# Performance work log

Hardware: AMD Instinct MI355X
Metric: run time of the kernel (lower is better)

The kernel has to match this reference:

```python
import jax, jax.numpy as jnp
import numpy as np


def setup_inputs() -> dict:
    key = jax.random.key(0)
    ks = jax.random.split(key, 5)
    B, Tm1, N, H = 128, 255, 256, 256  # batch, t-1, input_size, hidden_encoder
    X = jax.random.normal(ks[0], (B, Tm1, N), dtype=jnp.float32)
    W_attn = jax.random.normal(ks[1], (2 * H + Tm1, 1), dtype=jnp.float32) * 0.05
    b_attn = jnp.zeros((1,), dtype=jnp.float32)
    W_lstm = jax.random.normal(ks[2], (N, 4 * H), dtype=jnp.float32) * 0.05
    U_lstm = jax.random.normal(ks[3], (H, 4 * H), dtype=jnp.float32) * 0.05
    b_lstm = jnp.zeros((4 * H,), dtype=jnp.float32)
    return {"X": X, "W_attn": W_attn, "b_attn": b_attn,
            "W_lstm": W_lstm, "U_lstm": U_lstm, "b_lstm": b_lstm}


def reference(X, W_attn, b_attn, W_lstm, U_lstm, b_lstm):
    B, Tm1, N = X.shape
    H = U_lstm.shape[0]
    # init_state: RepeatVector(H)(X[:,0,:])[:,:,0] == X[:,0,0] tiled across hidden
    h0 = jnp.broadcast_to(X[:, 0, 0:1], (B, H))
    c0 = h0
    Xp = jnp.transpose(X, (0, 2, 1))  # (B, N, Tm1), reused every step

    def step(carry, x_t):  # x_t: (B, N) = X[:, t, :]
        h, c = carry
        # encoder_concat: (B, N, 2H + Tm1)
        feat = jnp.concatenate([
            jnp.broadcast_to(h[:, None, :], (B, N, H)),
            jnp.broadcast_to(c[:, None, :], (B, N, H)),
            Xp,
        ], axis=2)
        e = jnp.einsum('bnf,fo->bno', feat, W_attn)[..., 0] + b_attn[0]  # (B, N)
        alpha = jax.nn.softmax(e, axis=-1)  # softmax over input_size
        x_tilde = alpha * x_t  # (B, N)
        # Keras LSTM cell, gate order [i, f, g, o]
        z = x_tilde @ W_lstm + h @ U_lstm + b_lstm  # (B, 4H)
        i, f, g, o = jnp.split(z, 4, axis=-1)
        i = jax.nn.sigmoid(i)
        f = jax.nn.sigmoid(f)
        g = jnp.tanh(g)
        o = jax.nn.sigmoid(o)
        c_new = f * c + i * g
        h_new = o * jnp.tanh(c_new)
        return (h_new, c_new), (x_tilde, h_new)

    (_, _), (X_tilde, X_encoded) = jax.lax.scan(step, (h0, c0),
                                                jnp.transpose(X, (1, 0, 2)))
    X_tilde = jnp.transpose(X_tilde, (1, 0, 2))    # (B, Tm1, N)
    X_encoded = jnp.transpose(X_encoded, (1, 0, 2))  # (B, Tm1, H)
    return X_tilde, X_encoded
```

## Files before the change

kernel.cpp:

```cpp
#include <hip/hip_runtime.h>
#include <hip/hip_bf16.h>
#include <stdint.h>

#define B_ 128
#define T_ 255
#define N_ 256
#define H_ 256

#define RP_ 92
#define LQ_ 9

typedef _Float16 f16;
typedef _Float16 f16x2 __attribute__((ext_vector_type(2)));
typedef _Float16 f16x8 __attribute__((ext_vector_type(8)));
typedef float f32x4 __attribute__((ext_vector_type(4)));

static __device__ __forceinline__ float fdot2(uint32_t h, uint32_t u, float acc) {
#if __has_builtin(__builtin_amdgcn_fdot2)
  return __builtin_amdgcn_fdot2(__builtin_bit_cast(f16x2, h),
                                __builtin_bit_cast(f16x2, u), acc, false);
#else
  f16x2 a = __builtin_bit_cast(f16x2, h);
  f16x2 b = __builtin_bit_cast(f16x2, u);
  return acc + (float)a.x * (float)b.x + (float)a.y * (float)b.y;
#endif
}

__global__ __launch_bounds__(256) void k0_pack(const float* __restrict__ Wl,
                                               const float* __restrict__ Ul,
                                               uint32_t* __restrict__ u_packed,
                                               f16* __restrict__ wt) {
  int idx = blockIdx.x * 256 + threadIdx.x;
  if (idx < 256 * 1024) {
    int n = idx >> 8, k = idx & 255;
    wt[n * 256 + k] = (f16)Wl[k * 1024 + n];
  }
  if (idx < 128 * 1024) {
    int p = idx >> 10, c = idx & 1023;
    f16x2 v;
    v.x = (f16)Ul[(2 * p) * 1024 + c];
    v.y = (f16)Ul[(2 * p + 1) * 1024 + c];
    u_packed[idx] = __builtin_bit_cast(uint32_t, v);
  }
}

__global__ __launch_bounds__(256) void k1_alpha(const float* __restrict__ X,
                                                const float* __restrict__ Wa,
                                                float* __restrict__ alpha) {
  int b = blockIdx.x, n = threadIdx.x;
  const float* xb = X + b * (T_ * N_) + n;
  float a0 = 0.f, a1 = 0.f, a2 = 0.f, a3 = 0.f;
  int t = 0;
  for (; t + 4 <= T_; t += 4) {
    a0 += xb[(t + 0) * N_] * Wa[512 + t + 0];
    a1 += xb[(t + 1) * N_] * Wa[512 + t + 1];
    a2 += xb[(t + 2) * N_] * Wa[512 + t + 2];
    a3 += xb[(t + 3) * N_] * Wa[512 + t + 3];
  }
  for (; t < T_; ++t) a0 += xb[t * N_] * Wa[512 + t];
  float e = (a0 + a1) + (a2 + a3);

  __shared__ float red[4];
  float m = e;
  for (int off = 32; off > 0; off >>= 1) m = fmaxf(m, __shfl_xor(m, off));
  int wid = n >> 6;
  if ((n & 63) == 0) red[wid] = m;
  __syncthreads();
  m = fmaxf(fmaxf(red[0], red[1]), fmaxf(red[2], red[3]));
  float ex = __expf(e - m);
  float s = ex;
  for (int off = 32; off > 0; off >>= 1) s += __shfl_xor(s, off);
  __syncthreads();
  if ((n & 63) == 0) red[wid] = s;
  __syncthreads();
  s = (red[0] + red[1]) + (red[2] + red[3]);
  alpha[b * N_ + n] = ex / s;
}

__global__ __launch_bounds__(256) void k2_xtilde(const float4* __restrict__ X4,
                                                 const float* __restrict__ alpha,
                                                 float4* __restrict__ out4) {
  int i = blockIdx.x * 256 + threadIdx.x;
  if (i < B_ * T_ * 64) {
    int n4 = i & 63;
    int bt = i >> 6;
    int b = bt / T_;
    const float4* A4 = (const float4*)alpha;
    float4 x = X4[i], al = A4[b * 64 + n4];
    float4 r;
    r.x = x.x * al.x; r.y = x.y * al.y; r.z = x.z * al.z; r.w = x.w * al.w;
    out4[i] = r;
  }
}

#define LDA 40
__global__ __launch_bounds__(256, 2) void k3_gemm(const float* __restrict__ A,
                                                  const f16* __restrict__ Bt,
                                                  const float* __restrict__ bias,
                                                  f16* __restrict__ Cw) {
  __shared__ f16 As[128 * LDA];
  __shared__ f16 Bs[128 * LDA];
  int tid = threadIdx.x;
  int mt = blockIdx.x;
  int nt = blockIdx.y;
  int lane = tid & 63, wid = tid >> 6;
  int wm = (wid >> 1) * 64, wn = (wid & 1) * 64;
  f32x4 acc[4][4] = {};

  for (int k0 = 0; k0 < 256; k0 += 32) {
    __syncthreads();
#pragma unroll
    for (int it = 0; it < 4; ++it) {
      int idx = tid + it * 256;
      int r = idx >> 3, q = idx & 7;
      float4 v = *(const float4*)(A + (mt * 128 + r) * 256 + k0 + q * 4);
      f16x2 p0, p1;
      p0.x = (f16)v.x; p0.y = (f16)v.y; p1.x = (f16)v.z; p1.y = (f16)v.w;
      uint2 w;
      w.x = __builtin_bit_cast(uint32_t, p0);
      w.y = __builtin_bit_cast(uint32_t, p1);
      *(uint2*)(&As[r * LDA + q * 4]) = w;
    }
#pragma unroll
    for (int it = 0; it < 2; ++it) {
      int idx = tid + it * 256;
      int r = idx >> 2, q = idx & 3;
      uint4 v = *(const uint4*)(Bt + (nt * 128 + r) * 256 + k0 + q * 8);
      *(uint4*)(&Bs[r * LDA + q * 8]) = v;
    }
    __syncthreads();
    int kb = (lane >> 4) * 8;
    f16x8 af[4], bf[4];
#pragma unroll
    for (int i = 0; i < 4; ++i)
      af[i] = *(const f16x8*)(&As[(wm + i * 16 + (lane & 15)) * LDA + kb]);
#pragma unroll
    for (int j = 0; j < 4; ++j)
      bf[j] = *(const f16x8*)(&Bs[(wn + j * 16 + (lane & 15)) * LDA + kb]);
#pragma unroll
    for (int i = 0; i < 4; ++i)
#pragma unroll
      for (int j = 0; j < 4; ++j)
        acc[i][j] = __builtin_amdgcn_mfma_f32_16x16x32_f16(af[i], bf[j], acc[i][j], 0, 0, 0);
  }
  int colL = wn + (lane & 15);
  int rowB = wm + (lane >> 4) * 4;
#pragma unroll
  for (int j = 0; j < 4; ++j) {
    int ng = nt * 128 + colL + j * 16;
    float bv = bias[ng];
#pragma unroll
    for (int i = 0; i < 4; ++i)
#pragma unroll
      for (int r = 0; r < 4; ++r) {
        int mg = mt * 128 + rowB + i * 16 + r;
        Cw[mg * 1024 + ng] = (f16)(acc[i][j][r] + bv);
      }
  }
}

__global__ __launch_bounds__(1024) void k4_recur(const float* __restrict__ X,
                                                 const uint32_t* __restrict__ u_packed,
                                                 const f16* __restrict__ xwf,
                                                 float* __restrict__ Xenc) {
  __shared__ __align__(16) uint32_t u_lds[LQ_ * 1024 * 4];
  __shared__ __align__(16) f16 h_lds[256];
  __shared__ __align__(16) float z_lds[1024];
  int tid = threadIdx.x, b = blockIdx.x;

  uint32_t ur[RP_];
#pragma unroll
  for (int p = 0; p < RP_; ++p) ur[p] = u_packed[p * 1024 + tid];

  {
    uint4* dst = (uint4*)u_lds;
#pragma unroll
    for (int q = 0; q < LQ_; ++q) {
      int base = (RP_ + 4 * q) * 1024 + tid;
      uint4 v;
      v.x = u_packed[base];
      v.y = u_packed[base + 1024];
      v.z = u_packed[base + 2048];
      v.w = u_packed[base + 3072];
      dst[q * 1024 + tid] = v;
    }
  }
  float x00 = X[b * (T_ * N_)];
  float c_st = x00;
  if (tid < 256) h_lds[tid] = (f16)x00;
  __syncthreads();

  const f16* xwb = xwf + (size_t)b * T_ * 1024;
  float* encb = Xenc + (size_t)b * T_ * N_;
  const uint4* h4 = (const uint4*)h_lds;
  const uint4* u4 = (const uint4*)u_lds;

  float xwv = (float)xwb[tid];
  for (int t = 0; t < T_; ++t) {
    float xw_nxt = 0.f;
    if (t + 1 < T_) xw_nxt = (float)xwb[(t + 1) * 1024 + tid];

    float za = xwv, zb = 0.f;
#pragma unroll
    for (int q = 0; q < RP_ / 4; ++q) {
      uint4 hh = h4[q];
      za = fdot2(hh.x, ur[4 * q + 0], za);
      zb = fdot2(hh.y, ur[4 * q + 1], zb);
      za = fdot2(hh.z, ur[4 * q + 2], za);
      zb = fdot2(hh.w, ur[4 * q + 3], zb);
    }
#pragma unroll
    for (int q = 0; q < LQ_; ++q) {
      uint4 hh = h4[RP_ / 4 + q];
      uint4 uu = u4[q * 1024 + tid];
      za = fdot2(hh.x, uu.x, za);
      zb = fdot2(hh.y, uu.y, zb);
      za = fdot2(hh.z, uu.z, za);
      zb = fdot2(hh.w, uu.w, zb);
    }
    z_lds[tid] = za + zb;
    __syncthreads();
    if (tid < 256) {
      float zi = z_lds[tid], zf = z_lds[256 + tid];
      float zg = z_lds[512 + tid], zo = z_lds[768 + tid];
      float ig = 1.f / (1.f + __expf(-zi));
      float fg = 1.f / (1.f + __expf(-zf));
      float gg = 1.f - 2.f / (1.f + __expf(2.f * zg));
      float og = 1.f / (1.f + __expf(-zo));
      c_st = fg * c_st + ig * gg;
      float hv = og * (1.f - 2.f / (1.f + __expf(2.f * c_st)));
      encb[t * 256 + tid] = hv;
      h_lds[tid] = (f16)hv;
    }
    __syncthreads();
    xwv = xw_nxt;
  }
}

extern "C" void kernel_launch(void* const* d_in, const int* in_sizes, int n_in,
                              void* d_out, int out_size, void* d_ws, size_t ws_size,
                              hipStream_t stream) {
  const float* X = (const float*)d_in[0];
  const float* Wa = (const float*)d_in[1];
  const float* Wl = (const float*)d_in[3];
  const float* Ul = (const float*)d_in[4];
  const float* bl = (const float*)d_in[5];
  float* out = (float*)d_out;
  uint8_t* ws = (uint8_t*)d_ws;

  float* alpha = (float*)ws;
  uint32_t* u_packed = (uint32_t*)(ws + 131072);
  f16* wt = (f16*)(ws + 655360);
  f16* xw = (f16*)(ws + 1179648);

  k0_pack<<<1024, 256, 0, stream>>>(Wl, Ul, u_packed, wt);
  k1_alpha<<<128, 256, 0, stream>>>(X, Wa, alpha);
  k2_xtilde<<<8160, 256, 0, stream>>>((const float4*)X, alpha, (float4*)out);
  dim3 g3(255, 8);
  k3_gemm<<<g3, 256, 0, stream>>>(out, wt, bl, xw);
  k4_recur<<<128, 1024, 0, stream>>>(X, u_packed, xw, out + 8355840);
}
```

Before: 575.5 us.

## Split recurrent matvec over K halves with two columns per thread

The recurrent LSTM kernel now has each thread handle two gate columns (n and n+512) over half of the hidden dimension. Each h value read from LDS is then reused for two dot products, which cuts LDS broadcast reads of h per FMA. The two K-half partial sums are combined in a larger z buffer during the gate update. The register-resident U slice changes from 92 to 96 packed words, and the LDS-resident remainder changes layout.

```diff
diff --git a/kernel.cpp b/kernel.cpp
--- a/kernel.cpp
+++ b/kernel.cpp
@@ -7,8 +7,8 @@
 #define N_ 256
 #define H_ 256
 
-#define RP_ 92
-#define LQ_ 9
+#define RP2 48
+#define LG2 4
 
 typedef _Float16 f16;
 typedef _Float16 f16x2 __attribute__((ext_vector_type(2)));
@@ -163,26 +163,31 @@
                                                  const uint32_t* __restrict__ u_packed,
                                                  const f16* __restrict__ xwf,
                                                  float* __restrict__ Xenc) {
-  __shared__ __align__(16) uint32_t u_lds[LQ_ * 1024 * 4];
+  __shared__ __align__(16) uint32_t u_lds[8 * 1024 * 4];
   __shared__ __align__(16) f16 h_lds[256];
-  __shared__ __align__(16) float z_lds[1024];
+  __shared__ __align__(16) float z_lds[2048];
   int tid = threadIdx.x, b = blockIdx.x;
-
-  uint32_t ur[RP_];
-#pragma unroll
-  for (int p = 0; p < RP_; ++p) ur[p] = u_packed[p * 1024 + tid];
-
+  int kh = tid >> 9, n2 = tid & 511;
+
+  uint32_t urA[RP2], urB[RP2];
+  int pbase = kh * 64;
+#pragma unroll
+  for (int p = 0; p < RP2; ++p) {
+    urA[p] = u_packed[(pbase + p) * 1024 + n2];
+    urB[p] = u_packed[(pbase + p) * 1024 + n2 + 512];
+  }
   {
     uint4* dst = (uint4*)u_lds;
 #pragma unroll
-    for (int q = 0; q < LQ_; ++q) {
-      int base = (RP_ + 4 * q) * 1024 + tid;
+    for (int pl = 0; pl < 2 * LG2; ++pl) {
+      int kh2 = pl & 1, g = pl >> 1;
+      int bp = kh2 * 64 + RP2 + 4 * g;
       uint4 v;
-      v.x = u_packed[base];
-      v.y = u_packed[base + 1024];
-      v.z = u_packed[base + 2048];
-      v.w = u_packed[base + 3072];
-      dst[q * 1024 + tid] = v;
+      v.x = u_packed[(bp + 0) * 1024 + tid];
+      v.y = u_packed[(bp + 1) * 1024 + tid];
+      v.z = u_packed[(bp + 2) * 1024 + tid];
+      v.w = u_packed[(bp + 3) * 1024 + tid];
+      dst[pl * 1024 + tid] = v;
     }
   }
   float x00 = X[b * (T_ * N_)];
@@ -200,29 +205,42 @@
     float xw_nxt = 0.f;
     if (t + 1 < T_) xw_nxt = (float)xwb[(t + 1) * 1024 + tid];
 
-    float za = xwv, zb = 0.f;
-#pragma unroll
-    for (int q = 0; q < RP_ / 4; ++q) {
-      uint4 hh = h4[q];
-      za = fdot2(hh.x, ur[4 * q + 0], za);
-      zb = fdot2(hh.y, ur[4 * q + 1], zb);
-      za = fdot2(hh.z, ur[4 * q + 2], za);
-      zb = fdot2(hh.w, ur[4 * q + 3], zb);
-    }
-#pragma unroll
-    for (int q = 0; q < LQ_; ++q) {
-      uint4 hh = h4[RP_ / 4 + q];
-      uint4 uu = u4[q * 1024 + tid];
-      za = fdot2(hh.x, uu.x, za);
-      zb = fdot2(hh.y, uu.y, zb);
-      za = fdot2(hh.z, uu.z, za);
-      zb = fdot2(hh.w, uu.w, zb);
-    }
-    z_lds[tid] = za + zb;
+    float zA0 = (kh == 0) ? xwv : 0.f, zA1 = 0.f;
+    float zB0 = (kh == 0) ? 0.f : xwv, zB1 = 0.f;
+#pragma unroll
+    for (int g = 0; g < RP2 / 4; ++g) {
+      uint4 hh = h4[kh * 16 + g];
+      zA0 = fdot2(hh.x, urA[4 * g + 0], zA0);
+      zA1 = fdot2(hh.y, urA[4 * g + 1], zA1);
+      zA0 = fdot2(hh.z, urA[4 * g + 2], zA0);
+      zA1 = fdot2(hh.w, urA[4 * g + 3], zA1);
+      zB0 = fdot2(hh.x, urB[4 * g + 0], zB0);
+      zB1 = fdot2(hh.y, urB[4 * g + 1], zB1);
+      zB0 = fdot2(hh.z, urB[4 * g + 2], zB0);
+      zB1 = fdot2(hh.w, urB[4 * g + 3], zB1);
+    }
+#pragma unroll
+    for (int g = 0; g < LG2; ++g) {
+      uint4 hh = h4[kh * 16 + RP2 / 4 + g];
+      uint4 uA = u4[(g * 2 + kh) * 1024 + n2];
+      uint4 uB = u4[(g * 2 + kh) * 1024 + n2 + 512];
+      zA0 = fdot2(hh.x, uA.x, zA0);
+      zA1 = fdot2(hh.y, uA.y, zA1);
+      zA0 = fdot2(hh.z, uA.z, zA0);
+      zA1 = fdot2(hh.w, uA.w, zA1);
+      zB0 = fdot2(hh.x, uB.x, zB0);
+      zB1 = fdot2(hh.y, uB.y, zB1);
+      zB0 = fdot2(hh.z, uB.z, zB0);
+      zB1 = fdot2(hh.w, uB.w, zB1);
+    }
+    z_lds[kh * 1024 + n2] = zA0 + zA1;
+    z_lds[kh * 1024 + n2 + 512] = zB0 + zB1;
     __syncthreads();
     if (tid < 256) {
-      float zi = z_lds[tid], zf = z_lds[256 + tid];
-      float zg = z_lds[512 + tid], zo = z_lds[768 + tid];
+      float zi = z_lds[tid] + z_lds[1024 + tid];
+      float zf = z_lds[256 + tid] + z_lds[1280 + tid];
+      float zg = z_lds[512 + tid] + z_lds[1536 + tid];
+      float zo = z_lds[768 + tid] + z_lds[1792 + tid];
       float ig = 1.f / (1.f + __expf(-zi));
       float fg = 1.f / (1.f + __expf(-zf));
       float gg = 1.f - 2.f / (1.f + __expf(2.f * zg));
```

Result: faster. 543.3 us (-5.6%).

## Split recurrence K across lane quads with DPP reduction and single barrier

Applied to the files above, without the earlier changes.

Each hidden unit now belongs to a quad of four lanes. Each lane covers a quarter of the K range for all four gates, and the partial sums are reduced with DPP quad adds instead of going through a z buffer in LDS. Every lane then computes the gate nonlinearities redundantly, which removes one of the two barriers per timestep and the serial 256-thread gate phase. h is double-buffered in a padded LDS layout. The cost is redundant transcendental work in every lane and a changed split of weights between registers and LDS.

```diff
diff --git a/kernel.cpp b/kernel.cpp
--- a/kernel.cpp
+++ b/kernel.cpp
@@ -7,8 +7,7 @@
 #define N_ 256
 #define H_ 256
 
-#define RP_ 92
-#define LQ_ 9
+#define UR_ 24
 
 typedef _Float16 f16;
 typedef _Float16 f16x2 __attribute__((ext_vector_type(2)));
@@ -24,6 +23,13 @@
   f16x2 b = __builtin_bit_cast(f16x2, u);
   return acc + (float)a.x * (float)b.x + (float)a.y * (float)b.y;
 #endif
+}
+
+template <int CTRL>
+static __device__ __forceinline__ float dpp_qadd(float v) {
+  int x = __builtin_bit_cast(int, v);
+  int y = __builtin_amdgcn_update_dpp(0, x, CTRL, 0xF, 0xF, true);
+  return v + __builtin_bit_cast(float, y);
 }
 
 __global__ __launch_bounds__(256) void k0_pack(const float* __restrict__ Wl,
@@ -163,78 +169,121 @@
                                                  const uint32_t* __restrict__ u_packed,
                                                  const f16* __restrict__ xwf,
                                                  float* __restrict__ Xenc) {
-  __shared__ __align__(16) uint32_t u_lds[LQ_ * 1024 * 4];
-  __shared__ __align__(16) f16 h_lds[256];
-  __shared__ __align__(16) float z_lds[1024];
+  __shared__ __align__(16) uint4 u_lds[8][1024];
+  __shared__ __align__(16) f16 hrep[2][4 * 72];
   int tid = threadIdx.x, b = blockIdx.x;
-
-  uint32_t ur[RP_];
-#pragma unroll
-  for (int p = 0; p < RP_; ++p) ur[p] = u_packed[p * 1024 + tid];
-
-  {
-    uint4* dst = (uint4*)u_lds;
-#pragma unroll
-    for (int q = 0; q < LQ_; ++q) {
-      int base = (RP_ + 4 * q) * 1024 + tid;
-      uint4 v;
-      v.x = u_packed[base];
-      v.y = u_packed[base + 1024];
-      v.z = u_packed[base + 2048];
-      v.w = u_packed[base + 3072];
-      dst[q * 1024 + tid] = v;
-    }
-  }
+  int n = tid >> 2, kq = tid & 3;
+  int kb = kq * 32;
+
+  uint32_t ur0[UR_], ur1[UR_], ur2[UR_], ur3[UR_];
+#pragma unroll
+  for (int p = 0; p < UR_; ++p) {
+    ur0[p] = u_packed[(kb + p) * 1024 + n];
+    ur1[p] = u_packed[(kb + p) * 1024 + n + 256];
+    ur2[p] = u_packed[(kb + p) * 1024 + n + 512];
+    ur3[p] = u_packed[(kb + p) * 1024 + n + 768];
+  }
+#pragma unroll
+  for (int j = 0; j < 8; ++j) {
+    int c = j >> 1, a = j & 1;
+    int bp = kb + UR_ + 4 * a;
+    uint4 v;
+    v.x = u_packed[(bp + 0) * 1024 + n + c * 256];
+    v.y = u_packed[(bp + 1) * 1024 + n + c * 256];
+    v.z = u_packed[(bp + 2) * 1024 + n + c * 256];
+    v.w = u_packed[(bp + 3) * 1024 + n + c * 256];
+    u_lds[j][tid] = v;
+  }
+
   float x00 = X[b * (T_ * N_)];
   float c_st = x00;
-  if (tid < 256) h_lds[tid] = (f16)x00;
+  if (kq == (n >> 6)) hrep[0][kq * 72 + (n & 63)] = (f16)x00;
   __syncthreads();
 
   const f16* xwb = xwf + (size_t)b * T_ * 1024;
   float* encb = Xenc + (size_t)b * T_ * N_;
-  const uint4* h4 = (const uint4*)h_lds;
-  const uint4* u4 = (const uint4*)u_lds;
-
-  float xwv = (float)xwb[tid];
+  int xcol = n + (kq << 8);
+
+  float xwv = (float)xwb[xcol];
+  float hv_prev = 0.f;
   for (int t = 0; t < T_; ++t) {
-    float xw_nxt = 0.f;
-    if (t + 1 < T_) xw_nxt = (float)xwb[(t + 1) * 1024 + tid];
-
-    float za = xwv, zb = 0.f;
-#pragma unroll
-    for (int q = 0; q < RP_ / 4; ++q) {
-      uint4 hh = h4[q];
-      za = fdot2(hh.x, ur[4 * q + 0], za);
-      zb = fdot2(hh.y, ur[4 * q + 1], zb);
-      za = fdot2(hh.z, ur[4 * q + 2], za);
-      zb = fdot2(hh.w, ur[4 * q + 3], zb);
+    if (t > 0 && kq == 0) encb[(t - 1) * 256 + n] = hv_prev;
+    float xn = 0.f;
+    if (t + 1 < T_) xn = (float)xwb[(t + 1) * 1024 + xcol];
+
+    const uint4* h4 = (const uint4*)&hrep[t & 1][0];
+    int hbase = kq * 9;
+
+    float z0 = (kq == 0) ? xwv : 0.f;
+    float z1 = (kq == 1) ? xwv : 0.f;
+    float z2 = (kq == 2) ? xwv : 0.f;
+    float z3 = (kq == 3) ? xwv : 0.f;
+#pragma unroll
+    for (int g = 0; g < 6; ++g) {
+      uint4 hh = h4[hbase + g];
+      z0 = fdot2(hh.x, ur0[4 * g + 0], z0);
+      z1 = fdot2(hh.x, ur1[4 * g + 0], z1);
+      z2 = fdot2(hh.x, ur2[4 * g + 0], z2);
+      z3 = fdot2(hh.x, ur3[4 * g + 0], z3);
+      z0 = fdot2(hh.y, ur0[4 * g + 1], z0);
+      z1 = fdot2(hh.y, ur1[4 * g + 1], z1);
+      z2 = fdot2(hh.y, ur2[4 * g + 1], z2);
+      z3 = fdot2(hh.y, ur3[4 * g + 1], z3);
+      z0 = fdot2(hh.z, ur0[4 * g + 2], z0);
+      z1 = fdot2(hh.z, ur1[4 * g + 2], z1);
+      z2 = fdot2(hh.z, ur2[4 * g + 2], z2);
+      z3 = fdot2(hh.z, ur3[4 * g + 2], z3);
+      z0 = fdot2(hh.w, ur0[4 * g + 3], z0);
+      z1 = fdot2(hh.w, ur1[4 * g + 3], z1);
+      z2 = fdot2(hh.w, ur2[4 * g + 3], z2);
+      z3 = fdot2(hh.w, ur3[4 * g + 3], z3);
     }
-#pragma unroll
-    for (int q = 0; q < LQ_; ++q) {
-      uint4 hh = h4[RP_ / 4 + q];
-      uint4 uu = u4[q * 1024 + tid];
-      za = fdot2(hh.x, uu.x, za);
-      zb = fdot2(hh.y, uu.y, zb);
-      za = fdot2(hh.z, uu.z, za);
-      zb = fdot2(hh.w, uu.w, zb);
+    {
+      uint4 h6 = h4[hbase + 6];
+      uint4 h7 = h4[hbase + 7];
+      uint4 u;
+      u = u_lds[0][tid];
+      z0 = fdot2(h6.x, u.x, z0); z0 = fdot2(h6.y, u.y, z0);
+      z0 = fdot2(h6.z, u.z, z0); z0 = fdot2(h6.w, u.w, z0);
+      u = u_lds[1][tid];
+      z0 = fdot2(h7.x, u.x, z0); z0 = fdot2(h7.y, u.y, z0);
+      z0 = fdot2(h7.z, u.z, z0); z0 = fdot2(h7.w, u.w, z0);
+      u = u_lds[2][tid];
+      z1 = fdot2(h6.x, u.x, z1); z1 = fdot2(h6.y, u.y, z1);
+      z1 = fdot2(h6.z, u.z, z1); z1 = fdot2(h6.w, u.w, z1);
+      u = u_lds[3][tid];
+      z1 = fdot2(h7.x, u.x, z1); z1 = fdot2(h7.y, u.y, z1);
+      z1 = fdot2(h7.z, u.z, z1); z1 = fdot2(h7.w, u.w, z1);
+      u = u_lds[4][tid];
+      z2 = fdot2(h6.x, u.x, z2); z2 = fdot2(h6.y, u.y, z2);
+      z2 = fdot2(h6.z, u.z, z2); z2 = fdot2(h6.w, u.w, z2);
+      u = u_lds[5][tid];
+      z2 = fdot2(h7.x, u.x, z2); z2 = fdot2(h7.y, u.y, z2);
+      z2 = fdot2(h7.z, u.z, z2); z2 = fdot2(h7.w, u.w, z2);
+      u = u_lds[6][tid];
+      z3 = fdot2(h6.x, u.x, z3); z3 = fdot2(h6.y, u.y, z3);
+      z3 = fdot2(h6.z, u.z, z3); z3 = fdot2(h6.w, u.w, z3);
+      u = u_lds[7][tid];
+      z3 = fdot2(h7.x, u.x, z3); z3 = fdot2(h7.y, u.y, z3);
+      z3 = fdot2(h7.z, u.z, z3); z3 = fdot2(h7.w, u.w, z3);
     }
-    z_lds[tid] = za + zb;
+    z0 = dpp_qadd<0xB1>(z0); z1 = dpp_qadd<0xB1>(z1);
+    z2 = dpp_qadd<0xB1>(z2); z3 = dpp_qadd<0xB1>(z3);
+    z0 = dpp_qadd<0x4E>(z0); z1 = dpp_qadd<0x4E>(z1);
+    z2 = dpp_qadd<0x4E>(z2); z3 = dpp_qadd<0x4E>(z3);
+
+    float ig = 1.f / (1.f + __expf(-z0));
+    float fg = 1.f / (1.f + __expf(-z1));
+    float gg = 1.f - 2.f / (1.f + __expf(2.f * z2));
+    float og = 1.f / (1.f + __expf(-z3));
+    c_st = fg * c_st + ig * gg;
+    float hv = og * (1.f - 2.f / (1.f + __expf(2.f * c_st)));
+    hv_prev = hv;
+    if (kq == (n >> 6)) hrep[(t + 1) & 1][kq * 72 + (n & 63)] = (f16)hv;
     __syncthreads();
-    if (tid < 256) {
-      float zi = z_lds[tid], zf = z_lds[256 + tid];
-      float zg = z_lds[512 + tid], zo = z_lds[768 + tid];
-      float ig = 1.f / (1.f + __expf(-zi));
-      float fg = 1.f / (1.f + __expf(-zf));
-      float gg = 1.f - 2.f / (1.f + __expf(2.f * zg));
-      float og = 1.f / (1.f + __expf(-zo));
-      c_st = fg * c_st + ig * gg;
-      float hv = og * (1.f - 2.f / (1.f + __expf(2.f * c_st)));
-      encb[t * 256 + tid] = hv;
-      h_lds[tid] = (f16)hv;
-    }
-    __syncthreads();
-    xwv = xw_nxt;
-  }
+    xwv = xn;
+  }
+  if (kq == 0) encb[(T_ - 1) * 256 + n] = hv_prev;
 }
 
 extern "C" void kernel_launch(void* const* d_in, const int* in_sizes, int n_in,
```

After: 602.4 us. 1.05x slower.

## Split recurrent matvec over K so each thread reuses h across four gates

Applied to the files above, without the earlier changes.

Each of the 1024 threads in the recurrence kernel now owns one hidden column across all four gates and a quarter of the K range, instead of one full gate column over all of K. Every h value read from LDS is reused for four gate dot products, which cuts h broadcast reads from 32 to 8 uint4 per thread per step. The U slice is still split between registers (24 pairs per gate) and LDS (8 pairs per gate). The cost is a cross-thread reduction of four partial sums per gate through LDS before the activations, and slightly more registers per thread.

```diff
diff --git a/kernel.cpp b/kernel.cpp
--- a/kernel.cpp
+++ b/kernel.cpp
@@ -7,8 +7,7 @@
 #define N_ 256
 #define H_ 256
 
-#define RP_ 92
-#define LQ_ 9
+#define URQ 24
 
 typedef _Float16 f16;
 typedef _Float16 f16x2 __attribute__((ext_vector_type(2)));
@@ -163,26 +162,32 @@
                                                  const uint32_t* __restrict__ u_packed,
                                                  const f16* __restrict__ xwf,
                                                  float* __restrict__ Xenc) {
-  __shared__ __align__(16) uint32_t u_lds[LQ_ * 1024 * 4];
+  __shared__ __align__(16) uint32_t u_lds[8 * 1024 * 4];
   __shared__ __align__(16) f16 h_lds[256];
-  __shared__ __align__(16) float z_lds[1024];
+  __shared__ __align__(16) uint4 z4[4 * 256];
   int tid = threadIdx.x, b = blockIdx.x;
-
-  uint32_t ur[RP_];
-#pragma unroll
-  for (int p = 0; p < RP_; ++p) ur[p] = u_packed[p * 1024 + tid];
+  int kq = tid >> 8, n1 = tid & 255;
+  int pb = kq * 32;
+
+  uint32_t ur[4][URQ];
+#pragma unroll
+  for (int g = 0; g < 4; ++g)
+#pragma unroll
+    for (int p = 0; p < URQ; ++p)
+      ur[g][p] = u_packed[(pb + p) * 1024 + g * 256 + n1];
 
   {
     uint4* dst = (uint4*)u_lds;
 #pragma unroll
-    for (int q = 0; q < LQ_; ++q) {
-      int base = (RP_ + 4 * q) * 1024 + tid;
+    for (int pl = 0; pl < 8; ++pl) {
+      int g = pl >> 1, j = pl & 1;
+      int bp = pb + URQ + 4 * j;
       uint4 v;
-      v.x = u_packed[base];
-      v.y = u_packed[base + 1024];
-      v.z = u_packed[base + 2048];
-      v.w = u_packed[base + 3072];
-      dst[q * 1024 + tid] = v;
+      v.x = u_packed[(bp + 0) * 1024 + g * 256 + n1];
+      v.y = u_packed[(bp + 1) * 1024 + g * 256 + n1];
+      v.z = u_packed[(bp + 2) * 1024 + g * 256 + n1];
+      v.w = u_packed[(bp + 3) * 1024 + g * 256 + n1];
+      dst[pl * 1024 + tid] = v;
     }
   }
   float x00 = X[b * (T_ * N_)];
@@ -200,34 +205,84 @@
     float xw_nxt = 0.f;
     if (t + 1 < T_) xw_nxt = (float)xwb[(t + 1) * 1024 + tid];
 
-    float za = xwv, zb = 0.f;
-#pragma unroll
-    for (int q = 0; q < RP_ / 4; ++q) {
-      uint4 hh = h4[q];
-      za = fdot2(hh.x, ur[4 * q + 0], za);
-      zb = fdot2(hh.y, ur[4 * q + 1], zb);
-      za = fdot2(hh.z, ur[4 * q + 2], za);
-      zb = fdot2(hh.w, ur[4 * q + 3], zb);
-    }
-#pragma unroll
-    for (int q = 0; q < LQ_; ++q) {
-      uint4 hh = h4[RP_ / 4 + q];
-      uint4 uu = u4[q * 1024 + tid];
-      za = fdot2(hh.x, uu.x, za);
-      zb = fdot2(hh.y, uu.y, zb);
-      za = fdot2(hh.z, uu.z, za);
-      zb = fdot2(hh.w, uu.w, zb);
-    }
-    z_lds[tid] = za + zb;
+    float z0 = (kq == 0) ? xwv : 0.f;
+    float z1 = (kq == 1) ? xwv : 0.f;
+    float z2 = (kq == 2) ? xwv : 0.f;
+    float z3 = (kq == 3) ? xwv : 0.f;
+#pragma unroll
+    for (int j = 0; j < 2; ++j) {
+      uint4 u0 = u4[(0 * 2 + j) * 1024 + tid];
+      uint4 u1 = u4[(1 * 2 + j) * 1024 + tid];
+      uint4 u2 = u4[(2 * 2 + j) * 1024 + tid];
+      uint4 u3 = u4[(3 * 2 + j) * 1024 + tid];
+#pragma unroll
+      for (int gg = 0; gg < 3; ++gg) {
+        int c = j * 3 + gg;
+        uint4 hh = h4[kq * 8 + c];
+        z0 = fdot2(hh.x, ur[0][4 * c + 0], z0);
+        z1 = fdot2(hh.x, ur[1][4 * c + 0], z1);
+        z2 = fdot2(hh.x, ur[2][4 * c + 0], z2);
+        z3 = fdot2(hh.x, ur[3][4 * c + 0], z3);
+        z0 = fdot2(hh.y, ur[0][4 * c + 1], z0);
+        z1 = fdot2(hh.y, ur[1][4 * c + 1], z1);
+        z2 = fdot2(hh.y, ur[2][4 * c + 1], z2);
+        z3 = fdot2(hh.y, ur[3][4 * c + 1], z3);
+        z0 = fdot2(hh.z, ur[0][4 * c + 2], z0);
+        z1 = fdot2(hh.z, ur[1][4 * c + 2], z1);
+        z2 = fdot2(hh.z, ur[2][4 * c + 2], z2);
+        z3 = fdot2(hh.z, ur[3][4 * c + 2], z3);
+        z0 = fdot2(hh.w, ur[0][4 * c + 3], z0);
+        z1 = fdot2(hh.w, ur[1][4 * c + 3], z1);
+        z2 = fdot2(hh.w, ur[2][4 * c + 3], z2);
+        z3 = fdot2(hh.w, ur[3][4 * c + 3], z3);
+      }
+      {
+        uint4 hh = h4[kq * 8 + 6 + j];
+        z0 = fdot2(hh.x, u0.x, z0);
+        z1 = fdot2(hh.x, u1.x, z1);
+        z2 = fdot2(hh.x, u2.x, z2);
+        z3 = fdot2(hh.x, u3.x, z3);
+        z0 = fdot2(hh.y, u0.y, z0);
+        z1 = fdot2(hh.y, u1.y, z1);
+        z2 = fdot2(hh.y, u2.y, z2);
+        z3 = fdot2(hh.y, u3.y, z3);
+        z0 = fdot2(hh.z, u0.z, z0);
+        z1 = fdot2(hh.z, u1.z, z1);
+        z2 = fdot2(hh.z, u2.z, z2);
+        z3 = fdot2(hh.z, u3.z, z3);
+        z0 = fdot2(hh.w, u0.w, z0);
+        z1 = fdot2(hh.w, u1.w, z1);
+        z2 = fdot2(hh.w, u2.w, z2);
+        z3 = fdot2(hh.w, u3.w, z3);
+      }
+    }
+    {
+      uint4 zw;
+      zw.x = __builtin_bit_cast(uint32_t, z0);
+      zw.y = __builtin_bit_cast(uint32_t, z1);
+      zw.z = __builtin_bit_cast(uint32_t, z2);
+      zw.w = __builtin_bit_cast(uint32_t, z3);
+      z4[kq * 256 + n1] = zw;
+    }
     __syncthreads();
     if (tid < 256) {
-      float zi = z_lds[tid], zf = z_lds[256 + tid];
-      float zg = z_lds[512 + tid], zo = z_lds[768 + tid];
+      uint4 p0 = z4[tid];
+      uint4 p1 = z4[256 + tid];
+      uint4 p2 = z4[512 + tid];
+      uint4 p3 = z4[768 + tid];
+      float zi = (__builtin_bit_cast(float, p0.x) + __builtin_bit_cast(float, p1.x)) +
+                 (__builtin_bit_cast(float, p2.x) + __builtin_bit_cast(float, p3.x));
+      float zf = (__builtin_bit_cast(float, p0.y) + __builtin_bit_cast(float, p1.y)) +
+                 (__builtin_bit_cast(float, p2.y) + __builtin_bit_cast(float, p3.y));
+      float zg = (__builtin_bit_cast(float, p0.z) + __builtin_bit_cast(float, p1.z)) +
+                 (__builtin_bit_cast(float, p2.z) + __builtin_bit_cast(float, p3.z));
+      float zo = (__builtin_bit_cast(float, p0.w) + __builtin_bit_cast(float, p1.w)) +
+                 (__builtin_bit_cast(float, p2.w) + __builtin_bit_cast(float, p3.w));
       float ig = 1.f / (1.f + __expf(-zi));
       float fg = 1.f / (1.f + __expf(-zf));
-      float gg = 1.f - 2.f / (1.f + __expf(2.f * zg));
+      float gv = 1.f - 2.f / (1.f + __expf(2.f * zg));
       float og = 1.f / (1.f + __expf(-zo));
-      c_st = fg * c_st + ig * gg;
+      c_st = fg * c_st + ig * gv;
       float hv = og * (1.f - 2.f / (1.f + __expf(2.f * c_st)));
       encb[t * 256 + tid] = hv;
       h_lds[tid] = (f16)hv;
```

Measured after the change: 607.7 us. 5.6% more time.
